# Kernel tuning notes

Measured on AMD Instinct MI355X. Metric: run time of the kernel, lower is better.

## Reference

```python
import jax, jax.numpy as jnp
import numpy as np

B, S, D, H = 4, 2048, 512, 8
DK = D // H  # 64


def setup_inputs() -> dict:
    key = jax.random.key(0)
    ks = jax.random.split(key, 7)
    return {
        "q": jax.random.normal(ks[0], (B, S, D), dtype=jnp.float32),
        "k": jax.random.normal(ks[1], (B, S, D), dtype=jnp.float32),
        "v": jax.random.normal(ks[2], (B, S, D), dtype=jnp.float32),
        # per-head query projection weights (also used for k and v, replicating
        # the source's bug where q_linear projects all three inputs)
        "Wq": jax.random.normal(ks[3], (H, DK, D), dtype=jnp.float32) * (1.0 / np.sqrt(D)),
        "bq": jax.random.normal(ks[4], (H, DK), dtype=jnp.float32) * 0.02,
        "Wout": jax.random.normal(ks[5], (D, H * DK), dtype=jnp.float32) * (1.0 / np.sqrt(D)),
        "bout": jax.random.normal(ks[6], (D,), dtype=jnp.float32) * 0.02,
    }


def reference(q, k, v, Wq, bq, Wout, bout):
    # Per-head projections, batched over heads. NOTE: the original module
    # (buggy but faithful) applies the SAME q_linear to q, k and v.
    scale = 1.0 / jnp.sqrt(jnp.asarray(Wq.shape[1], dtype=q.dtype))
    qh = jnp.einsum("bsd,hed->bhse", q, Wq) + bq[:, None, :]  # [B,H,S,DK]
    kh = jnp.einsum("bsd,hed->bhse", k, Wq) + bq[:, None, :]
    vh = jnp.einsum("bsd,hed->bhse", v, Wq) + bq[:, None, :]
    scores = jnp.einsum("bhqe,bhke->bhqk", qh, kh) * scale  # [B,H,S,S]
    weights = jax.nn.softmax(scores, axis=-1)
    heads = jnp.einsum("bhqk,bhke->bhqe", weights, vh)  # [B,H,S,DK]
    # concat heads along feature dim (head-major order matches torch.cat)
    concat = heads.transpose(0, 2, 1, 3).reshape(q.shape[0], q.shape[1], -1)
    return concat @ Wout.T + bout
```

## Files before the change

kernel.cpp:

```cpp
#include <hip/hip_runtime.h>

#define BB 4
#define SS 2048
#define DD 512
#define HH 8
#define DKK 64
#define HDK 512

typedef __attribute__((ext_vector_type(4))) float f32x4;
typedef __attribute__((ext_vector_type(8))) __bf16 bf16x8;
typedef __attribute__((ext_vector_type(4))) __bf16 bf16x4;

#define MFMA16(a, b, c) __builtin_amdgcn_mfma_f32_16x16x32_bf16((a), (b), (c), 0, 0, 0)

#define GLOAD_LDS16(gptr, lptr)                                                    \
    __builtin_amdgcn_global_load_lds(                                              \
        (const __attribute__((address_space(1))) void*)(gptr),                     \
        (__attribute__((address_space(3))) void*)(lptr), 16, 0, 0)

__device__ inline bf16x8 cvt48(const f32x4 f0, const f32x4 f1) {
    bf16x8 w;
    w[0] = (__bf16)f0[0]; w[1] = (__bf16)f0[1]; w[2] = (__bf16)f0[2]; w[3] = (__bf16)f0[3];
    w[4] = (__bf16)f1[0]; w[5] = (__bf16)f1[1]; w[6] = (__bf16)f1[2]; w[7] = (__bf16)f1[3];
    return w;
}

__global__ __launch_bounds__(256) void proj_kernel(
    const float* __restrict__ q, const float* __restrict__ k, const float* __restrict__ v,
    const float* __restrict__ Wq, const float* __restrict__ bq,
    __bf16* __restrict__ qh, __bf16* __restrict__ kh, __bf16* __restrict__ vt)
{
    const int z  = blockIdx.z;
    const float* X = (z == 0) ? q : (z == 1) ? k : v;
    const int m0 = blockIdx.x * 128;
    const int n0 = blockIdx.y * 128;

    __shared__ __align__(16) float As[128 * 64];
    __shared__ __align__(16) float Bs[128 * 64];

    const int t    = threadIdx.x;
    const int lane = t & 63, wid = t >> 6;
    const int lo   = lane & 15, hi = lane >> 4;
    const int wm   = wid >> 1, wn = wid & 1;

    const int srofs  = lane >> 4;
    const int schunk = lane & 15;

    f32x4 acc[4][4] = {};

    for (int k0 = 0; k0 < DD; k0 += 64) {
        __syncthreads();
#pragma unroll
        for (int i = 0; i < 8; ++i) {
            const int r0  = 32 * wid + 4 * i;
            const int row = r0 + srofs;
            const int gco = ((schunk ^ (row & 7)) << 4);
            GLOAD_LDS16((const char*)&X [(size_t)(m0 + row) * DD + k0] + gco,
                        (char*)As + r0 * 256);
            GLOAD_LDS16((const char*)&Wq[(size_t)(n0 + row) * DD + k0] + gco,
                        (char*)Bs + r0 * 256);
        }
        __syncthreads();

#pragma unroll
        for (int kk = 0; kk < 2; ++kk) {
            bf16x8 a[4], b[4];
#pragma unroll
            for (int mi = 0; mi < 4; ++mi) {
                const int ar = wm * 64 + mi * 16 + lo;
                const int rs = (ar & 7) << 4;
                const int cb = kk * 128 + hi * 32;
                f32x4 f0 = *reinterpret_cast<const f32x4*>((const char*)As + ar * 256 + (cb ^ rs));
                f32x4 f1 = *reinterpret_cast<const f32x4*>((const char*)As + ar * 256 + ((cb + 16) ^ rs));
                a[mi] = cvt48(f0, f1);
            }
#pragma unroll
            for (int ni = 0; ni < 4; ++ni) {
                const int br = wn * 64 + ni * 16 + lo;
                const int rs = (br & 7) << 4;
                const int cb = kk * 128 + hi * 32;
                f32x4 f0 = *reinterpret_cast<const f32x4*>((const char*)Bs + br * 256 + (cb ^ rs));
                f32x4 f1 = *reinterpret_cast<const f32x4*>((const char*)Bs + br * 256 + ((cb + 16) ^ rs));
                b[ni] = cvt48(f0, f1);
            }
#pragma unroll
            for (int mi = 0; mi < 4; ++mi)
#pragma unroll
                for (int ni = 0; ni < 4; ++ni)
                    acc[mi][ni] = MFMA16(a[mi], b[ni], acc[mi][ni]);
        }
    }

#pragma unroll
    for (int mi = 0; mi < 4; ++mi) {
#pragma unroll
        for (int ni = 0; ni < 4; ++ni) {
            const int n = n0 + wn * 64 + ni * 16 + lo;
            const float bias = bq[n];
            const int h_ = n >> 6, e_ = n & 63;
#pragma unroll
            for (int r = 0; r < 4; ++r) {
                const int m = m0 + wm * 64 + mi * 16 + hi * 4 + r;
                const float val = acc[mi][ni][r] + bias;
                const int b_ = m >> 11, s_ = m & (SS - 1);
                const size_t bh = (size_t)(b_ * HH + h_);
                if (z == 0)
                    qh[(bh * SS + s_) * DKK + e_] = (__bf16)val;
                else if (z == 1)
                    kh[(bh * SS + s_) * DKK + e_] = (__bf16)val;
                else
                    vt[(bh * DKK + e_) * SS + s_] = (__bf16)val;
            }
        }
    }
}

__global__ __launch_bounds__(256) void attn_kernel(
    const __bf16* __restrict__ qh, const __bf16* __restrict__ kh,
    const __bf16* __restrict__ vt, __bf16* __restrict__ concat)
{
    const int q0 = blockIdx.x * 64;
    const int bh = blockIdx.y;
    const int b_ = bh >> 3, h_ = bh & 7;
    const size_t base = (size_t)bh * SS * DKK;
    const __bf16* qhp = qh + base;
    const __bf16* khp = kh + base;
    const __bf16* vtp = vt + base;

    const int t    = threadIdx.x;
    const int lane = t & 63, wid = t >> 6;
    const int lo   = lane & 15, hi = lane >> 4;

    __shared__ __align__(16) __bf16 Ks[64 * 64];
    __shared__ __align__(16) __bf16 Vts[64 * 64];
    __shared__ __align__(16) __bf16 Ps[4][16][72];

    char* KsB  = (char*)Ks;
    char* VtsB = (char*)Vts;

    const int sr   = lane >> 3;
    const int gcb  = (lane & 7) << 4;
    const int scb  = gcb ^ (sr << 4);
    const int srow = 16 * wid + sr;

    bf16x8 qf[2];
#pragma unroll
    for (int kk = 0; kk < 2; ++kk)
        qf[kk] = *reinterpret_cast<const bf16x8*>(
            &qhp[(size_t)(q0 + 16 * wid + lo) * DKK + 32 * kk + 8 * hi]);

    f32x4 acc[4] = {};
    float m_run = -INFINITY, l_run = 0.f;

    for (int kv0 = 0; kv0 < SS; kv0 += 64) {
        bf16x8 kr0 = *reinterpret_cast<const bf16x8*>(
            (const char*)&khp[(size_t)(kv0 + srow) * DKK] + gcb);
        bf16x8 kr1 = *reinterpret_cast<const bf16x8*>(
            (const char*)&khp[(size_t)(kv0 + srow + 8) * DKK] + gcb);
        bf16x8 vr0 = *reinterpret_cast<const bf16x8*>(
            (const char*)&vtp[(size_t)srow * SS + kv0] + gcb);
        bf16x8 vr1 = *reinterpret_cast<const bf16x8*>(
            (const char*)&vtp[(size_t)(srow + 8) * SS + kv0] + gcb);

        __syncthreads();
        *reinterpret_cast<bf16x8*>(KsB  + srow * 128 + scb)       = kr0;
        *reinterpret_cast<bf16x8*>(KsB  + (srow + 8) * 128 + scb) = kr1;
        *reinterpret_cast<bf16x8*>(VtsB + srow * 128 + scb)       = vr0;
        *reinterpret_cast<bf16x8*>(VtsB + (srow + 8) * 128 + scb) = vr1;
        __syncthreads();

        f32x4 sc[4] = {};
#pragma unroll
        for (int kk = 0; kk < 2; ++kk) {
            bf16x8 kf[4];
#pragma unroll
            for (int f = 0; f < 4; ++f) {
                const int row = 16 * f + lo;
                const int cb  = (64 * kk + 16 * hi) ^ ((row & 7) << 4);
                kf[f] = *reinterpret_cast<const bf16x8*>(KsB + row * 128 + cb);
            }
#pragma unroll
            for (int f = 0; f < 4; ++f)
                sc[f] = MFMA16(kf[f], qf[kk], sc[f]);
        }

        {
            float mx = -1e30f;
#pragma unroll
            for (int f = 0; f < 4; ++f)
#pragma unroll
                for (int r = 0; r < 4; ++r)
                    mx = fmaxf(mx, sc[f][r]);
            mx = fmaxf(mx, __shfl_xor(mx, 16));
            mx = fmaxf(mx, __shfl_xor(mx, 32));
            const float mnew = fmaxf(m_run, mx * 0.125f);
            const float scl  = __expf(m_run - mnew);
            float rs = 0.f;
#pragma unroll
            for (int f = 0; f < 4; ++f) {
                bf16x4 pk;
#pragma unroll
                for (int r = 0; r < 4; ++r) {
                    const float e = __expf(fmaf(sc[f][r], 0.125f, -mnew));
                    rs += e;
                    pk[r] = (__bf16)e;
                }
                *reinterpret_cast<bf16x4*>(&Ps[wid][lo][16 * f + 4 * hi]) = pk;
            }
            rs += __shfl_xor(rs, 16);
            rs += __shfl_xor(rs, 32);
            l_run = l_run * scl + rs;
            m_run = mnew;
#pragma unroll
            for (int f = 0; f < 4; ++f)
                acc[f] *= scl;
        }

#pragma unroll
        for (int kk = 0; kk < 2; ++kk) {
            bf16x8 pb = *reinterpret_cast<const bf16x8*>(&Ps[wid][lo][32 * kk + 8 * hi]);
#pragma unroll
            for (int f = 0; f < 4; ++f) {
                const int row = 16 * f + lo;
                const int cb  = (64 * kk + 16 * hi) ^ ((row & 7) << 4);
                bf16x8 vf = *reinterpret_cast<const bf16x8*>(VtsB + row * 128 + cb);
                acc[f] = MFMA16(vf, pb, acc[f]);
            }
        }
    }

    {
        const float inv = 1.0f / l_run;
        const int qrow = q0 + 16 * wid + lo;
        const size_t ob = ((size_t)b_ * SS + qrow) * HDK + h_ * DKK;
#pragma unroll
        for (int f = 0; f < 4; ++f) {
            bf16x4 o;
#pragma unroll
            for (int r = 0; r < 4; ++r)
                o[r] = (__bf16)(acc[f][r] * inv);
            *reinterpret_cast<bf16x4*>(&concat[ob + 16 * f + 4 * hi]) = o;
        }
    }
}

__global__ __launch_bounds__(256) void outproj_kernel(
    const __bf16* __restrict__ concat, const float* __restrict__ Wout,
    const float* __restrict__ bout, float* __restrict__ out)
{
    const int m0 = blockIdx.x * 128;
    const int n0 = blockIdx.y * 128;

    __shared__ __align__(16) __bf16 As[128 * 64];
    __shared__ __align__(16) float  Bs[128 * 64];

    const int t    = threadIdx.x;
    const int lane = t & 63, wid = t >> 6;
    const int lo   = lane & 15, hi = lane >> 4;
    const int wm   = wid >> 1, wn = wid & 1;

    f32x4 acc[4][4] = {};

    for (int k0 = 0; k0 < HDK; k0 += 64) {
        __syncthreads();
#pragma unroll
        for (int i = 0; i < 4; ++i) {
            const int r0  = 32 * wid + 8 * i;
            const int row = r0 + (lane >> 3);
            const int gco = ((lane & 7) ^ (row & 7)) << 4;
            GLOAD_LDS16((const char*)&concat[(size_t)(m0 + row) * HDK + k0] + gco,
                        (char*)As + r0 * 128);
        }
#pragma unroll
        for (int i = 0; i < 8; ++i) {
            const int r0  = 32 * wid + 4 * i;
            const int row = r0 + (lane >> 4);
            const int gco = ((lane & 15) ^ (row & 7)) << 4;
            GLOAD_LDS16((const char*)&Wout[(size_t)(n0 + row) * HDK + k0] + gco,
                        (char*)Bs + r0 * 256);
        }
        __syncthreads();

#pragma unroll
        for (int kk = 0; kk < 2; ++kk) {
            bf16x8 a[4], b[4];
#pragma unroll
            for (int mi = 0; mi < 4; ++mi) {
                const int ar = wm * 64 + mi * 16 + lo;
                const int cb = (kk * 64 + hi * 16) ^ ((ar & 7) << 4);
                a[mi] = *reinterpret_cast<const bf16x8*>((const char*)As + ar * 128 + cb);
            }
#pragma unroll
            for (int ni = 0; ni < 4; ++ni) {
                const int br = wn * 64 + ni * 16 + lo;
                const int rs = (br & 7) << 4;
                const int cb = kk * 128 + hi * 32;
                f32x4 f0 = *reinterpret_cast<const f32x4*>((const char*)Bs + br * 256 + (cb ^ rs));
                f32x4 f1 = *reinterpret_cast<const f32x4*>((const char*)Bs + br * 256 + ((cb + 16) ^ rs));
                b[ni] = cvt48(f0, f1);
            }
#pragma unroll
            for (int mi = 0; mi < 4; ++mi)
#pragma unroll
                for (int ni = 0; ni < 4; ++ni)
                    acc[mi][ni] = MFMA16(a[mi], b[ni], acc[mi][ni]);
        }
    }

#pragma unroll
    for (int mi = 0; mi < 4; ++mi) {
#pragma unroll
        for (int ni = 0; ni < 4; ++ni) {
            const int n = n0 + wn * 64 + ni * 16 + lo;
            const float bias = bout[n];
#pragma unroll
            for (int r = 0; r < 4; ++r) {
                const int m = m0 + wm * 64 + mi * 16 + hi * 4 + r;
                out[(size_t)m * DD + n] = acc[mi][ni][r] + bias;
            }
        }
    }
}

extern "C" void kernel_launch(void* const* d_in, const int* in_sizes, int n_in,
                              void* d_out, int out_size, void* d_ws, size_t ws_size,
                              hipStream_t stream)
{
    (void)in_sizes; (void)n_in; (void)out_size; (void)ws_size;
    const float* q    = (const float*)d_in[0];
    const float* k    = (const float*)d_in[1];
    const float* v    = (const float*)d_in[2];
    const float* Wq   = (const float*)d_in[3];
    const float* bq   = (const float*)d_in[4];
    const float* Wout = (const float*)d_in[5];
    const float* bout = (const float*)d_in[6];
    float* out = (float*)d_out;

    char* ws = (char*)d_ws;
    __bf16* qh = (__bf16*)(ws);
    __bf16* kh = (__bf16*)(ws + (8u << 20));
    __bf16* vt = (__bf16*)(ws + (16u << 20));
    __bf16* cc = (__bf16*)(ws + (24u << 20));

    proj_kernel<<<dim3(BB * SS / 128, HDK / 128, 3), 256, 0, stream>>>(q, k, v, Wq, bq, qh, kh, vt);
    attn_kernel<<<dim3(SS / 64, BB * HH), 256, 0, stream>>>(qh, kh, vt, cc);
    outproj_kernel<<<dim3(BB * SS / 128, DD / 128), 256, 0, stream>>>(cc, Wout, bout, out);
}
```

Measured before the change: 223.8 us.

## Pre-convert weights to bf16 and double-buffer projection GEMM tiles

```diff
diff --git a/kernel.cpp b/kernel.cpp
--- a/kernel.cpp
+++ b/kernel.cpp
@@ -25,70 +25,93 @@
     return w;
 }
 
+__global__ __launch_bounds__(256) void wconv_kernel(
+    const float* __restrict__ Wq, const float* __restrict__ Wout,
+    __bf16* __restrict__ Wqb, __bf16* __restrict__ Wob)
+{
+    const int tid = blockIdx.x * 256 + threadIdx.x;
+    const float* src;
+    __bf16* dst;
+    int off;
+    if (tid < 32768) { src = Wq;   dst = Wqb; off = tid * 8; }
+    else             { src = Wout; dst = Wob; off = (tid - 32768) * 8; }
+    f32x4 f0 = *reinterpret_cast<const f32x4*>(src + off);
+    f32x4 f1 = *reinterpret_cast<const f32x4*>(src + off + 4);
+    *reinterpret_cast<bf16x8*>(dst + off) = cvt48(f0, f1);
+}
+
 __global__ __launch_bounds__(256) void proj_kernel(
     const float* __restrict__ q, const float* __restrict__ k, const float* __restrict__ v,
-    const float* __restrict__ Wq, const float* __restrict__ bq,
+    const __bf16* __restrict__ Wqb, const float* __restrict__ bq,
     __bf16* __restrict__ qh, __bf16* __restrict__ kh, __bf16* __restrict__ vt)
 {
     const int z  = blockIdx.z;
     const float* X = (z == 0) ? q : (z == 1) ? k : v;
-    const int m0 = blockIdx.x * 128;
-    const int n0 = blockIdx.y * 128;
-
-    __shared__ __align__(16) float As[128 * 64];
-    __shared__ __align__(16) float Bs[128 * 64];
+    const int n0 = blockIdx.x * 128;
+    const int m0 = blockIdx.y * 128;
+
+    __shared__ __align__(16) float  As[2][128 * 32];
+    __shared__ __align__(16) __bf16 Bs[2][128 * 32];
 
     const int t    = threadIdx.x;
     const int lane = t & 63, wid = t >> 6;
     const int lo   = lane & 15, hi = lane >> 4;
     const int wm   = wid >> 1, wn = wid & 1;
 
-    const int srofs  = lane >> 4;
-    const int schunk = lane & 15;
+    const int alr  = lane >> 3;
+    const int achk = ((lane & 7) ^ alr) << 4;
+    const char* aSrc = (const char*)(X + (size_t)(m0 + 32 * wid + alr) * DD) + achk;
+    const int blr  = lane >> 2;
+    const int bchk = ((lane & 3) ^ ((lane >> 3) & 3)) << 4;
+    const char* bSrc = (const char*)(Wqb + (size_t)(n0 + 32 * wid + blr) * DD) + bchk;
 
     f32x4 acc[4][4] = {};
 
-    for (int k0 = 0; k0 < DD; k0 += 64) {
+    auto stage = [&](int buf, int tt) {
+#pragma unroll
+        for (int i = 0; i < 4; ++i)
+            GLOAD_LDS16(aSrc + (size_t)i * (8 * DD * 4) + (size_t)tt * 128,
+                        (char*)As[buf] + (32 * wid + 8 * i) * 128);
+#pragma unroll
+        for (int i = 0; i < 2; ++i)
+            GLOAD_LDS16(bSrc + (size_t)i * (16 * DD * 2) + (size_t)tt * 64,
+                        (char*)Bs[buf] + (32 * wid + 16 * i) * 64);
+    };
+    auto compute = [&](int buf) {
+        bf16x8 a[4], b[4];
+#pragma unroll
+        for (int mi = 0; mi < 4; ++mi) {
+            const int ar = wm * 64 + mi * 16 + lo;
+            const int sw = (ar & 7);
+            f32x4 f0 = *reinterpret_cast<const f32x4*>(
+                (const char*)As[buf] + ar * 128 + (((2 * hi) ^ sw) << 4));
+            f32x4 f1 = *reinterpret_cast<const f32x4*>(
+                (const char*)As[buf] + ar * 128 + (((2 * hi + 1) ^ sw) << 4));
+            a[mi] = cvt48(f0, f1);
+        }
+#pragma unroll
+        for (int ni = 0; ni < 4; ++ni) {
+            const int br = wn * 64 + ni * 16 + lo;
+            const int cb = (hi ^ ((lo >> 1) & 3)) << 4;
+            b[ni] = *reinterpret_cast<const bf16x8*>((const char*)Bs[buf] + br * 64 + cb);
+        }
+        __builtin_amdgcn_s_setprio(1);
+#pragma unroll
+        for (int mi = 0; mi < 4; ++mi)
+#pragma unroll
+            for (int ni = 0; ni < 4; ++ni)
+                acc[mi][ni] = MFMA16(a[mi], b[ni], acc[mi][ni]);
+        __builtin_amdgcn_s_setprio(0);
+    };
+
+    stage(0, 0);
+    __syncthreads();
+    int cur = 0;
+    for (int tt = 0; tt < 16; ++tt) {
+        if (tt < 15) stage(cur ^ 1, tt + 1);
+        compute(cur);
         __syncthreads();
-#pragma unroll
-        for (int i = 0; i < 8; ++i) {
-            const int r0  = 32 * wid + 4 * i;
-            const int row = r0 + srofs;
-            const int gco = ((schunk ^ (row & 7)) << 4);
-            GLOAD_LDS16((const char*)&X [(size_t)(m0 + row) * DD + k0] + gco,
-                        (char*)As + r0 * 256);
-            GLOAD_LDS16((const char*)&Wq[(size_t)(n0 + row) * DD + k0] + gco,
-                        (char*)Bs + r0 * 256);
-        }
-        __syncthreads();
-
-#pragma unroll
-        for (int kk = 0; kk < 2; ++kk) {
-            bf16x8 a[4], b[4];
-#pragma unroll
-            for (int mi = 0; mi < 4; ++mi) {
-                const int ar = wm * 64 + mi * 16 + lo;
-                const int rs = (ar & 7) << 4;
-                const int cb = kk * 128 + hi * 32;
-                f32x4 f0 = *reinterpret_cast<const f32x4*>((const char*)As + ar * 256 + (cb ^ rs));
-                f32x4 f1 = *reinterpret_cast<const f32x4*>((const char*)As + ar * 256 + ((cb + 16) ^ rs));
-                a[mi] = cvt48(f0, f1);
-            }
-#pragma unroll
-            for (int ni = 0; ni < 4; ++ni) {
-                const int br = wn * 64 + ni * 16 + lo;
-                const int rs = (br & 7) << 4;
-                const int cb = kk * 128 + hi * 32;
-                f32x4 f0 = *reinterpret_cast<const f32x4*>((const char*)Bs + br * 256 + (cb ^ rs));
-                f32x4 f1 = *reinterpret_cast<const f32x4*>((const char*)Bs + br * 256 + ((cb + 16) ^ rs));
-                b[ni] = cvt48(f0, f1);
-            }
-#pragma unroll
-            for (int mi = 0; mi < 4; ++mi)
-#pragma unroll
-                for (int ni = 0; ni < 4; ++ni)
-                    acc[mi][ni] = MFMA16(a[mi], b[ni], acc[mi][ni]);
-        }
+        cur ^= 1;
     }
 
 #pragma unroll
@@ -245,66 +268,66 @@
 }
 
 __global__ __launch_bounds__(256) void outproj_kernel(
-    const __bf16* __restrict__ concat, const float* __restrict__ Wout,
+    const __bf16* __restrict__ concat, const __bf16* __restrict__ Wob,
     const float* __restrict__ bout, float* __restrict__ out)
 {
-    const int m0 = blockIdx.x * 128;
-    const int n0 = blockIdx.y * 128;
-
-    __shared__ __align__(16) __bf16 As[128 * 64];
-    __shared__ __align__(16) float  Bs[128 * 64];
+    const int n0 = blockIdx.x * 128;
+    const int m0 = blockIdx.y * 128;
+
+    __shared__ __align__(16) __bf16 As[2][128 * 32];
+    __shared__ __align__(16) __bf16 Bs[2][128 * 32];
 
     const int t    = threadIdx.x;
     const int lane = t & 63, wid = t >> 6;
     const int lo   = lane & 15, hi = lane >> 4;
     const int wm   = wid >> 1, wn = wid & 1;
 
+    const int blr  = lane >> 2;
+    const int bchk = ((lane & 3) ^ ((lane >> 3) & 3)) << 4;
+    const char* aSrc = (const char*)(concat + (size_t)(m0 + 32 * wid + blr) * HDK) + bchk;
+    const char* bSrc = (const char*)(Wob    + (size_t)(n0 + 32 * wid + blr) * HDK) + bchk;
+
     f32x4 acc[4][4] = {};
 
-    for (int k0 = 0; k0 < HDK; k0 += 64) {
+    auto stage = [&](int buf, int tt) {
+#pragma unroll
+        for (int i = 0; i < 2; ++i) {
+            GLOAD_LDS16(aSrc + (size_t)i * (16 * HDK * 2) + (size_t)tt * 64,
+                        (char*)As[buf] + (32 * wid + 16 * i) * 64);
+            GLOAD_LDS16(bSrc + (size_t)i * (16 * HDK * 2) + (size_t)tt * 64,
+                        (char*)Bs[buf] + (32 * wid + 16 * i) * 64);
+        }
+    };
+    auto compute = [&](int buf) {
+        bf16x8 a[4], b[4];
+        const int cb = (hi ^ ((lo >> 1) & 3)) << 4;
+#pragma unroll
+        for (int mi = 0; mi < 4; ++mi) {
+            const int ar = wm * 64 + mi * 16 + lo;
+            a[mi] = *reinterpret_cast<const bf16x8*>((const char*)As[buf] + ar * 64 + cb);
+        }
+#pragma unroll
+        for (int ni = 0; ni < 4; ++ni) {
+            const int br = wn * 64 + ni * 16 + lo;
+            b[ni] = *reinterpret_cast<const bf16x8*>((const char*)Bs[buf] + br * 64 + cb);
+        }
+        __builtin_amdgcn_s_setprio(1);
+#pragma unroll
+        for (int mi = 0; mi < 4; ++mi)
+#pragma unroll
+            for (int ni = 0; ni < 4; ++ni)
+                acc[mi][ni] = MFMA16(a[mi], b[ni], acc[mi][ni]);
+        __builtin_amdgcn_s_setprio(0);
+    };
+
+    stage(0, 0);
+    __syncthreads();
+    int cur = 0;
+    for (int tt = 0; tt < 16; ++tt) {
+        if (tt < 15) stage(cur ^ 1, tt + 1);
+        compute(cur);
         __syncthreads();
-#pragma unroll
-        for (int i = 0; i < 4; ++i) {
-            const int r0  = 32 * wid + 8 * i;
-            const int row = r0 + (lane >> 3);
-            const int gco = ((lane & 7) ^ (row & 7)) << 4;
-            GLOAD_LDS16((const char*)&concat[(size_t)(m0 + row) * HDK + k0] + gco,
-                        (char*)As + r0 * 128);
-        }
-#pragma unroll
-        for (int i = 0; i < 8; ++i) {
-            const int r0  = 32 * wid + 4 * i;
-            const int row = r0 + (lane >> 4);
-            const int gco = ((lane & 15) ^ (row & 7)) << 4;
-            GLOAD_LDS16((const char*)&Wout[(size_t)(n0 + row) * HDK + k0] + gco,
-                        (char*)Bs + r0 * 256);
-        }
-        __syncthreads();
-
-#pragma unroll
-        for (int kk = 0; kk < 2; ++kk) {
-            bf16x8 a[4], b[4];
-#pragma unroll
-            for (int mi = 0; mi < 4; ++mi) {
-                const int ar = wm * 64 + mi * 16 + lo;
-                const int cb = (kk * 64 + hi * 16) ^ ((ar & 7) << 4);
-                a[mi] = *reinterpret_cast<const bf16x8*>((const char*)As + ar * 128 + cb);
-            }
-#pragma unroll
-            for (int ni = 0; ni < 4; ++ni) {
-                const int br = wn * 64 + ni * 16 + lo;
-                const int rs = (br & 7) << 4;
-                const int cb = kk * 128 + hi * 32;
-                f32x4 f0 = *reinterpret_cast<const f32x4*>((const char*)Bs + br * 256 + (cb ^ rs));
-                f32x4 f1 = *reinterpret_cast<const f32x4*>((const char*)Bs + br * 256 + ((cb + 16) ^ rs));
-                b[ni] = cvt48(f0, f1);
-            }
-#pragma unroll
-            for (int mi = 0; mi < 4; ++mi)
-#pragma unroll
-                for (int ni = 0; ni < 4; ++ni)
-                    acc[mi][ni] = MFMA16(a[mi], b[ni], acc[mi][ni]);
-        }
+        cur ^= 1;
     }
 
 #pragma unroll
@@ -337,12 +360,15 @@
     float* out = (float*)d_out;
 
     char* ws = (char*)d_ws;
-    __bf16* qh = (__bf16*)(ws);
-    __bf16* kh = (__bf16*)(ws + (8u << 20));
-    __bf16* vt = (__bf16*)(ws + (16u << 20));
-    __bf16* cc = (__bf16*)(ws + (24u << 20));
-
-    proj_kernel<<<dim3(BB * SS / 128, HDK / 128, 3), 256, 0, stream>>>(q, k, v, Wq, bq, qh, kh, vt);
+    __bf16* qh  = (__bf16*)(ws);
+    __bf16* kh  = (__bf16*)(ws + (8u << 20));
+    __bf16* vt  = (__bf16*)(ws + (16u << 20));
+    __bf16* cc  = (__bf16*)(ws + (24u << 20));
+    __bf16* Wqb = (__bf16*)(ws + (32u << 20));
+    __bf16* Wob = (__bf16*)(ws + (32u << 20) + (512u << 10));
+
+    wconv_kernel<<<256, 256, 0, stream>>>(Wq, Wout, Wqb, Wob);
+    proj_kernel<<<dim3(HDK / 128, BB * SS / 128, 3), 256, 0, stream>>>(q, k, v, Wqb, bq, qh, kh, vt);
     attn_kernel<<<dim3(SS / 64, BB * HH), 256, 0, stream>>>(qh, kh, vt, cc);
-    outproj_kernel<<<dim3(BB * SS / 128, DD / 128), 256, 0, stream>>>(cc, Wout, bout, out);
-}
+    outproj_kernel<<<dim3(DD / 128, BB * SS / 128), 256, 0, stream>>>(cc, Wob, bout, out);
+}
```

Result: faster. 213.1 us (-4.7%).
